# Kernel tuning notes

Measured on AMD Instinct MI355X. Metric: run time of the kernel, lower is better.

The kernel has to match this reference:

```python
import jax, jax.numpy as jnp
import numpy as np

B, C, H, W = 16, 128, 64, 64
LN_EPS = 1e-5


def _gru_dir(x, w_ih, w_hh, b_ih, b_hh, reverse):
    # x: [N, T, C]; PyTorch GRU cell math:
    # r = sig(Wir x + bir + Whr h + bhr); z = sig(Wiz x + biz + Whz h + bhz)
    xp = jnp.einsum('ntc,gc->ntg', x, w_ih) + b_ih  # [N,T,3C] precomputed input gates
    xs = jnp.swapaxes(xp, 0, 1)  # [T,N,3C]
    h0 = jnp.zeros((x.shape[0], w_hh.shape[1]), x.dtype)

    def step(h, xt):
        g = h @ w_hh.T + b_hh
        xr, xz, xn = jnp.split(xt, 3, axis=-1)
        hr, hz, hn = jnp.split(g, 3, axis=-1)
        r = jax.nn.sigmoid(xr + hr)
        z = jax.nn.sigmoid(xz + hz)
        n = jnp.tanh(xn + r * hn)
        h2 = (1.0 - z) * n + z * h
        return h2, h2

    _, ys = jax.lax.scan(step, h0, xs, reverse=reverse)
    return jnp.swapaxes(ys, 0, 1)  # [N,T,C]


def _gru_bidir(x, wih_f, whh_f, bih_f, bhh_f, wih_b, whh_b, bib_b, bhh_b):
    of = _gru_dir(x, wih_f, whh_f, bih_f, bhh_f, False)
    ob = _gru_dir(x, wih_b, whh_b, bib_b, bhh_b, True)
    return jnp.concatenate([of, ob], axis=-1)  # [N,T,2C]


def _forward(x, ln_g, ln_b,
             h_wih_f, h_whh_f, h_bih_f, h_bhh_f,
             h_wih_b, h_whh_b, h_bih_b, h_bhh_b,
             w_wih_f, w_whh_f, w_bih_f, w_bhh_f,
             w_wih_b, w_whh_b, w_bih_b, w_bhh_b,
             proj_w, proj_b):
    Bn, Cc, Hh, Ww = x.shape
    x_flat = x.reshape(Bn, Cc, Hh * Ww).transpose(0, 2, 1)  # b (h w) c
    mu = x_flat.mean(-1, keepdims=True)
    var = ((x_flat - mu) ** 2).mean(-1, keepdims=True)
    xn = (x_flat - mu) * jax.lax.rsqrt(var + LN_EPS) * ln_g + ln_b
    x4 = xn.reshape(Bn, Hh, Ww, Cc)
    # horizontal scan: rows as batch, sequence along W
    x_h = x4.reshape(Bn * Hh, Ww, Cc)
    out_h = _gru_bidir(x_h, h_wih_f, h_whh_f, h_bih_f, h_bhh_f,
                       h_wih_b, h_whh_b, h_bih_b, h_bhh_b)
    out_h = out_h.reshape(Bn, Hh * Ww, 2 * Cc)
    # vertical scan: cols as batch, sequence along H
    x_v = x4.transpose(0, 2, 1, 3).reshape(Bn * Ww, Hh, Cc)
    out_v = _gru_bidir(x_v, w_wih_f, w_whh_f, w_bih_f, w_bhh_f,
                       w_wih_b, w_whh_b, w_bih_b, w_bhh_b)
    out_v = out_v.reshape(Bn, Ww, Hh, 2 * Cc).transpose(0, 2, 1, 3).reshape(Bn, Hh * Ww, 2 * Cc)
    out = jnp.concatenate([out_h, out_v], axis=-1) @ proj_w.T + proj_b
    out = out + x_flat  # dropout in eval mode = identity
    return out.transpose(0, 2, 1).reshape(Bn, Cc, Hh, Ww)


def setup_inputs():
    key = jax.random.key(0)
    key, kx = jax.random.split(key)
    d = {
        'x': jax.random.normal(kx, (B, C, H, W), jnp.float32),
        'ln_g': jnp.ones((C,), jnp.float32),
        'ln_b': jnp.zeros((C,), jnp.float32),
    }
    bound = 1.0 / np.sqrt(C)  # torch GRU init: U(-1/sqrt(hidden), 1/sqrt(hidden))
    shapes = {'wih': (3 * C, C), 'whh': (3 * C, C), 'bih': (3 * C,), 'bhh': (3 * C,)}
    for pre in ('h', 'w'):
        for dr in ('f', 'b'):
            for p, sh in shapes.items():
                key, k1 = jax.random.split(key)
                d[f'{pre}_{p}_{dr}'] = jax.random.uniform(k1, sh, jnp.float32, -bound, bound)
    bp = 1.0 / np.sqrt(4 * C)
    key, k1, k2 = jax.random.split(key, 3)
    d['proj_w'] = jax.random.uniform(k1, (C, 4 * C), jnp.float32, -bp, bp)
    d['proj_b'] = jax.random.uniform(k2, (C,), jnp.float32, -bp, bp)
    return d


def reference(x, ln_g, ln_b,
              h_wih_f, h_whh_f, h_bih_f, h_bhh_f,
              h_wih_b, h_whh_b, h_bih_b, h_bhh_b,
              w_wih_f, w_whh_f, w_bih_f, w_bhh_f,
              w_wih_b, w_whh_b, w_bih_b, w_bhh_b,
              proj_w, proj_b):
    return _forward(x, ln_g, ln_b,
                    h_wih_f, h_whh_f, h_bih_f, h_bhh_f,
                    h_wih_b, h_whh_b, h_bih_b, h_bhh_b,
                    w_wih_f, w_whh_f, w_bih_f, w_bhh_f,
                    w_wih_b, w_whh_b, w_bih_b, w_bhh_b,
                    proj_w, proj_b)
```

## Files before the change

### kernel.cpp

```cpp
#include <hip/hip_runtime.h>

typedef short bf16x8 __attribute__((ext_vector_type(8)));
typedef float f32x4 __attribute__((ext_vector_type(4)));

static __device__ __forceinline__ unsigned short f2bf(float f) {
  unsigned u = __builtin_bit_cast(unsigned, f);
  u += 0x7FFFu + ((u >> 16) & 1u);
  return (unsigned short)(u >> 16);
}

static __device__ __forceinline__ bf16x8 pack8s(const float* p, float s) {
  float4 a = *(const float4*)p;
  float4 b = *(const float4*)(p + 4);
  bf16x8 r;
  r[0] = (short)f2bf(a.x * s); r[1] = (short)f2bf(a.y * s);
  r[2] = (short)f2bf(a.z * s); r[3] = (short)f2bf(a.w * s);
  r[4] = (short)f2bf(b.x * s); r[5] = (short)f2bf(b.y * s);
  r[6] = (short)f2bf(b.z * s); r[7] = (short)f2bf(b.w * s);
  return r;
}

#define NLOG2E -1.442695040888963f
#define N2LOG2E -2.885390081777927f

__global__ __launch_bounds__(512, 2) void ln_kernel(
    const float* __restrict__ x, const float* __restrict__ lg,
    const float* __restrict__ lb, unsigned short* __restrict__ xn,
    const float* __restrict__ pw, unsigned short* __restrict__ pwb) {
  __shared__ __align__(16) unsigned char slds[35840];
  float* mu_s = (float*)(slds + 34816);
  float* rs_s = (float*)(slds + 35328);
  const int tid = threadIdx.x;
  const int bid = blockIdx.x;
  if (bid < 128) {
    const int i = bid * 512 + tid;
    pwb[i] = f2bf(pw[i]);
  }
  const int b = bid >> 5;
  const int hw0 = (bid & 31) << 7;
  const int q = tid >> 5, slot = tid & 31;
  const int lane = tid & 63, wv = tid >> 6;

  const float* xbase = x + ((size_t)b * 128) * 4096 + hw0 + (slot << 2);
  float4 xv[8];
#pragma unroll
  for (int p = 0; p < 8; ++p)
    xv[p] = *(const float4*)(xbase + (size_t)(q * 8 + p) * 4096);

  float s1[4] = {0.f, 0.f, 0.f, 0.f}, s2[4] = {0.f, 0.f, 0.f, 0.f};
#pragma unroll
  for (int p = 0; p < 8; ++p) {
    s1[0] += xv[p].x; s2[0] = fmaf(xv[p].x, xv[p].x, s2[0]);
    s1[1] += xv[p].y; s2[1] = fmaf(xv[p].y, xv[p].y, s2[1]);
    s1[2] += xv[p].z; s2[2] = fmaf(xv[p].z, xv[p].z, s2[2]);
    s1[3] += xv[p].w; s2[3] = fmaf(xv[p].w, xv[p].w, s2[3]);
  }
#pragma unroll
  for (int j = 0; j < 4; ++j) {
    s1[j] += __shfl_xor(s1[j], 32);
    s2[j] += __shfl_xor(s2[j], 32);
  }
  if (lane < 32) {
    float* psp = (float*)(slds + (wv * 32 + slot) * 36);
#pragma unroll
    for (int j = 0; j < 4; ++j) { psp[j] = s1[j]; psp[4 + j] = s2[j]; }
  }
  __syncthreads();
  if (tid < 128) {
    const int sl2 = tid >> 2, j2 = tid & 3;
    float a1 = 0.f, a2 = 0.f;
#pragma unroll
    for (int w = 0; w < 8; ++w) {
      const float* psp = (const float*)(slds + (w * 32 + sl2) * 36);
      a1 += psp[j2]; a2 += psp[4 + j2];
    }
    const float mu = a1 * 0.0078125f;
    const float var = a2 * 0.0078125f - mu * mu;
    mu_s[tid] = mu;
    rs_s[tid] = rsqrtf(var + 1e-5f);
  }
  __syncthreads();

  float lgv[8], lbv[8];
#pragma unroll
  for (int p = 0; p < 8; ++p) { lgv[p] = lg[q * 8 + p]; lbv[p] = lb[q * 8 + p]; }
#pragma unroll
  for (int j = 0; j < 4; ++j) {
    const int pos = (slot << 2) + j;
    const float mu = mu_s[pos], rs = rs_s[pos];
    float y[8];
#pragma unroll
    for (int p = 0; p < 8; ++p) {
      const float xvj = j == 0 ? xv[p].x : j == 1 ? xv[p].y : j == 2 ? xv[p].z : xv[p].w;
      y[p] = (xvj - mu) * rs * lgv[p] + lbv[p];
    }
    unsigned h0, h1, h2, h3;
    asm("v_cvt_pk_bf16_f32 %0, %1, %2" : "=v"(h0) : "v"(y[0]), "v"(y[1]));
    asm("v_cvt_pk_bf16_f32 %0, %1, %2" : "=v"(h1) : "v"(y[2]), "v"(y[3]));
    asm("v_cvt_pk_bf16_f32 %0, %1, %2" : "=v"(h2) : "v"(y[4]), "v"(y[5]));
    asm("v_cvt_pk_bf16_f32 %0, %1, %2" : "=v"(h3) : "v"(y[6]), "v"(y[7]));
    uint4 v; v.x = h0; v.y = h1; v.z = h2; v.w = h3;
    *(uint4*)(slds + pos * 272 + (q << 4)) = v;
  }
  __syncthreads();
#pragma unroll
  for (int it = 0; it < 4; ++it) {
    const int idx = (it << 9) + tid;
    const int row = idx >> 4, g = idx & 15;
    uint4 v = *(const uint4*)(slds + row * 272 + (g << 4));
    *(uint4*)((unsigned char*)xn + ((size_t)(b * 4096 + hw0 + row)) * 256 + (g << 4)) = v;
  }
}

__global__ __launch_bounds__(512, 2) void scan_kernel(
    const unsigned short* __restrict__ xn, unsigned short* __restrict__ cat,
    const float* __restrict__ wih0, const float* __restrict__ whh0,
    const float* __restrict__ bih0, const float* __restrict__ bhh0,
    const float* __restrict__ wih1, const float* __restrict__ whh1,
    const float* __restrict__ bih1, const float* __restrict__ bhh1,
    const float* __restrict__ wih2, const float* __restrict__ whh2,
    const float* __restrict__ bih2, const float* __restrict__ bhh2,
    const float* __restrict__ wih3, const float* __restrict__ whh3,
    const float* __restrict__ bih3, const float* __restrict__ bhh3) {
  __shared__ __align__(16) unsigned char lds[16384];
  const int tid = threadIdx.x;
  const int bid = blockIdx.x;
  const int dir = bid >> 6;
  const int grp = bid & 63;
  const int fwd = !(dir & 1);
  const int vert = dir >> 1;
  const int b = grp >> 2;
  const int r0 = (grp & 3) << 4;
  const int wv = tid >> 6;
  const int lane = tid & 63;
  const int l15 = lane & 15;
  const int l4 = lane >> 4;

  const float* wih = dir == 0 ? wih0 : dir == 1 ? wih1 : dir == 2 ? wih2 : wih3;
  const float* whh = dir == 0 ? whh0 : dir == 1 ? whh1 : dir == 2 ? whh2 : whh3;
  const float* bih = dir == 0 ? bih0 : dir == 1 ? bih1 : dir == 2 ? bih2 : bih3;
  const float* bhh = dir == 0 ? bhh0 : dir == 1 ? bhh1 : dir == 2 ? bhh2 : bhh3;

  const int ca = (wv << 4) + l15;
  bf16x8 wf[3][2][4];
#pragma unroll
  for (int g = 0; g < 3; ++g) {
    const float sc = g == 2 ? N2LOG2E : NLOG2E;
#pragma unroll
    for (int s = 0; s < 2; ++s) {
      const float* Wp = s ? whh : wih;
#pragma unroll
      for (int kc = 0; kc < 4; ++kc)
        wf[g][s][kc] = pack8s(Wp + (size_t)((g << 7) + ca) * 128 + (kc << 5) + (l4 << 3), sc);
    }
  }
  const int cb = (wv << 4) + (l4 << 2);
  f32x4 br4, bz4, bnx4, bnh4;
  {
    float4 a = *(const float4*)(bih + cb), b2 = *(const float4*)(bhh + cb);
    br4[0] = (a.x + b2.x) * NLOG2E; br4[1] = (a.y + b2.y) * NLOG2E;
    br4[2] = (a.z + b2.z) * NLOG2E; br4[3] = (a.w + b2.w) * NLOG2E;
    a = *(const float4*)(bih + 128 + cb); b2 = *(const float4*)(bhh + 128 + cb);
    bz4[0] = (a.x + b2.x) * NLOG2E; bz4[1] = (a.y + b2.y) * NLOG2E;
    bz4[2] = (a.z + b2.z) * NLOG2E; bz4[3] = (a.w + b2.w) * NLOG2E;
    a = *(const float4*)(bih + 256 + cb);
    bnx4[0] = a.x * N2LOG2E; bnx4[1] = a.y * N2LOG2E;
    bnx4[2] = a.z * N2LOG2E; bnx4[3] = a.w * N2LOG2E;
    b2 = *(const float4*)(bhh + 256 + cb);
    bnh4[0] = b2.x * N2LOG2E; bnh4[1] = b2.y * N2LOG2E;
    bnh4[2] = b2.z * N2LOG2E; bnh4[3] = b2.w * N2LOG2E;
  }

  const int ss = tid >> 4, ck = tid & 15;
  const unsigned char* xsp =
      (const unsigned char*)xn +
      (vert ? ((size_t)b << 20) + (size_t)(r0 + ss) * 256 + (ck << 4)
            : ((size_t)(b * 64 + r0 + ss) << 14) + (ck << 4));
  const int xstep = vert ? 16384 : 256;
  const int sdst = (ss * 256 + (ck << 4)) ^ ((ss & 15) << 4);

  const int seq = r0 + l15;
  const int cstep = vert ? 65536 : 1024;
  unsigned char* catp =
      (unsigned char*)cat +
      ((size_t)b * 4096 + (size_t)(vert ? seq : seq * 64)) * 1024 + dir * 256 + (cb << 1) +
      (size_t)(fwd ? 0 : 63) * cstep;
  const int cdelta = fwd ? cstep : -cstep;

  *(unsigned long long*)(lds + 8192 + tid * 8) = 0ull;
  f32x4 hst = {0.f, 0.f, 0.f, 0.f};

  uint4 sX, sY;
  f32x4 grA, gzA, gnxA, grB, gzB, gnxB;
  {
    const unsigned char* xlq =
        (const unsigned char*)xn +
        (vert ? ((size_t)b << 20) + (size_t)(fwd ? 0 : 63) * 16384 + (size_t)seq * 256
              : ((size_t)(b * 64 + seq) << 14) + (size_t)(fwd ? 0 : 63) * 256) +
        (l4 << 4);
    bf16x8 x0[4];
#pragma unroll
    for (int kc = 0; kc < 4; ++kc) x0[kc] = *(const bf16x8*)(xlq + (kc << 6));
    uint4 s1v;
    if (tid < 256) {
      s1v = *(const uint4*)(xsp + (fwd ? 1 : 62) * xstep);
      sX = *(const uint4*)(xsp + (fwd ? 2 : 61) * xstep);
    }
    grA = br4; gzA = bz4; gnxA = bnx4;
#pragma unroll
    for (int kc = 0; kc < 4; ++kc) {
      grA = __builtin_amdgcn_mfma_f32_16x16x32_bf16(wf[0][0][kc], x0[kc], grA, 0, 0, 0);
      gzA = __builtin_amdgcn_mfma_f32_16x16x32_bf16(wf[1][0][kc], x0[kc], gzA, 0, 0, 0);
      gnxA = __builtin_amdgcn_mfma_f32_16x16x32_bf16(wf[2][0][kc], x0[kc], gnxA, 0, 0, 0);
    }
    if (tid < 256) *(uint4*)(lds + 4096 + sdst) = s1v;
  }
  __syncthreads();

#define STEP(TT, HCUR, HNXT, XRD, XWR, XW, XL, GRC, GZC, GNXC, GRN, GZN, GNXN)  \
  {                                                                             \
    bf16x8 ha[4], xa[4];                                                        \
    _Pragma("unroll")                                                           \
    for (int kc = 0; kc < 4; ++kc) {                                            \
      const int base = (l15 * 256 + (kc << 6) + (l4 << 4)) ^ (l15 << 4);        \
      ha[kc] = *(const bf16x8*)(lds + (HCUR) + base);                           \
      xa[kc] = *(const bf16x8*)(lds + (XRD) + base);                            \
    }                                                                           \
    if (tid < 256) {                                                            \
      *(uint4*)(lds + (XWR) + sdst) = XW;                                       \
      const int tl = (TT) + 3 > 63 ? 63 : (TT) + 3;                             \
      XL = *(const uint4*)(xsp + (fwd ? tl : 63 - tl) * xstep);                 \
    }                                                                           \
    f32x4 rh = {0.f, 0.f, 0.f, 0.f}, zh = {0.f, 0.f, 0.f, 0.f}, nh = bnh4;     \
    _Pragma("unroll")                                                           \
    for (int kc = 0; kc < 4; ++kc) {                                            \
      rh = __builtin_amdgcn_mfma_f32_16x16x32_bf16(wf[0][1][kc], ha[kc], rh, 0, 0, 0); \
      zh = __builtin_amdgcn_mfma_f32_16x16x32_bf16(wf[1][1][kc], ha[kc], zh, 0, 0, 0); \
      nh = __builtin_amdgcn_mfma_f32_16x16x32_bf16(wf[2][1][kc], ha[kc], nh, 0, 0, 0); \
    }                                                                           \
    GRN = br4; GZN = bz4; GNXN = bnx4;                                          \
    _Pragma("unroll")                                                           \
    for (int kc = 0; kc < 4; ++kc) {                                            \
      GRN = __builtin_amdgcn_mfma_f32_16x16x32_bf16(wf[0][0][kc], xa[kc], GRN, 0, 0, 0); \
      GZN = __builtin_amdgcn_mfma_f32_16x16x32_bf16(wf[1][0][kc], xa[kc], GZN, 0, 0, 0); \
      GNXN = __builtin_amdgcn_mfma_f32_16x16x32_bf16(wf[2][0][kc], xa[kc], GNXN, 0, 0, 0); \
    }                                                                           \
    f32x4 hnew;                                                                 \
    _Pragma("unroll")                                                           \
    for (int r = 0; r < 4; ++r) {                                               \
      const float er = __builtin_amdgcn_exp2f(GRC[r] + rh[r]);                  \
      const float rr = __builtin_amdgcn_rcpf(1.f + er);                         \
      const float ez = __builtin_amdgcn_exp2f(GZC[r] + zh[r]);                  \
      const float zz = __builtin_amdgcn_rcpf(1.f + ez);                         \
      const float pre = GNXC[r] + rr * nh[r];                                   \
      const float e2 = __builtin_amdgcn_exp2f(pre);                             \
      const float nn = fmaf(2.f, __builtin_amdgcn_rcpf(1.f + e2), -1.f);        \
      hnew[r] = nn + zz * (hst[r] - nn);                                        \
    }                                                                           \
    hst = hnew;                                                                 \
    unsigned hp0, hp1;                                                          \
    asm("v_cvt_pk_bf16_f32 %0, %1, %2" : "=v"(hp0) : "v"(hnew[0]), "v"(hnew[1])); \
    asm("v_cvt_pk_bf16_f32 %0, %1, %2" : "=v"(hp1) : "v"(hnew[2]), "v"(hnew[3])); \
    {                                                                           \
      unsigned long long hp = (unsigned long long)hp0 | ((unsigned long long)hp1 << 32); \
      *(unsigned long long*)(lds + (HNXT) + ((l15 * 256 + (cb << 1)) ^ (l15 << 4))) = hp; \
    }                                                                           \
    {                                                                           \
      uint2 v; v.x = hp0; v.y = hp1;                                            \
      *(uint2*)catp = v;                                                        \
      catp += cdelta;                                                           \
    }                                                                           \
    asm volatile("s_waitcnt lgkmcnt(0)" ::: "memory");                          \
    __builtin_amdgcn_s_barrier();                                               \
    asm volatile("" ::: "memory");                                              \
  }

  for (int tt2 = 0; tt2 < 64; tt2 += 2) {
    STEP(tt2, 8192, 12288, 4096, 0, sX, sY, grA, gzA, gnxA, grB, gzB, gnxB);
    STEP(tt2 + 1, 12288, 8192, 0, 4096, sY, sX, grB, gzB, gnxB, grA, gzA, gnxA);
  }
#undef STEP
}

__global__ __launch_bounds__(512, 4) void proj_kernel(
    const unsigned short* __restrict__ cat, const unsigned short* __restrict__ pwb,
    const float* __restrict__ pb, const float* __restrict__ x,
    float* __restrict__ out) {
  __shared__ __align__(16) unsigned char lds[33280];
  const int tid = threadIdx.x;
  const int bid = blockIdx.x;
  const int row0 = bid << 6;
  const int b = row0 >> 12;
  const int hw0 = row0 & 4095;
  const int wv = tid >> 6, lane = tid & 63, l15 = lane & 15, l4 = lane >> 4;

  const int cc = (wv << 4) + l15;
  bf16x8 wfr[16];
#pragma unroll
  for (int kc = 0; kc < 16; ++kc)
    wfr[kc] = *(const bf16x8*)(pwb + (size_t)cc * 512 + (kc << 5) + (l4 << 3));
  const float pbv = pb[cc];

  f32x4 acc[4];
#pragma unroll
  for (int mt = 0; mt < 4; ++mt) acc[mt] = {pbv, pbv, pbv, pbv};

#pragma unroll
  for (int s = 0; s < 2; ++s) {
#pragma unroll
    for (int it = 0; it < 4; ++it) {
      const int item = tid + (it << 9);
      const int rr = item >> 6, ckk = item & 63;
      uint4 v = *(const uint4*)((const unsigned char*)cat +
                                ((size_t)(row0 + (s << 5) + rr)) * 1024 + ckk * 16);
      *(uint4*)(lds + rr * 1024 + ((ckk ^ (rr & 7)) << 4)) = v;
    }
    __syncthreads();
#pragma unroll
    for (int mh = 0; mh < 2; ++mh) {
      const int mt = (s << 1) + mh;
      const int rl = (mh << 4) + l15;
#pragma unroll
      for (int kc = 0; kc < 16; ++kc) {
        bf16x8 af =
            *(const bf16x8*)(lds + rl * 1024 + ((((kc << 2) + l4) ^ (rl & 7)) << 4));
        acc[mt] = __builtin_amdgcn_mfma_f32_16x16x32_bf16(af, wfr[kc], acc[mt], 0, 0, 0);
      }
    }
    __syncthreads();
  }

#pragma unroll
  for (int mt = 0; mt < 4; ++mt)
#pragma unroll
    for (int j = 0; j < 4; ++j)
      *(float*)(lds + cc * 260 + (((mt << 4) + (l4 << 2) + j) << 2)) = acc[mt][j];
  __syncthreads();
#pragma unroll
  for (int it = 0; it < 16; ++it) {
    const int c = (wv << 4) + it;
    const float v = *(const float*)(lds + c * 260 + (lane << 2));
    const size_t off = (size_t)(b * 128 + c) * 4096 + hw0 + lane;
    out[off] = v + x[off];
  }
}

extern "C" void kernel_launch(void* const* d_in, const int* in_sizes, int n_in,
                              void* d_out, int out_size, void* d_ws, size_t ws_size,
                              hipStream_t stream) {
  const float* x = (const float*)d_in[0];
  const float* lg = (const float*)d_in[1];
  const float* lb = (const float*)d_in[2];
  unsigned short* xn = (unsigned short*)d_ws;
  unsigned short* cat =
      (unsigned short*)((unsigned char*)d_ws + 16777216);
  unsigned short* pwb =
      (unsigned short*)((unsigned char*)d_ws + 16777216 + 67108864);

  ln_kernel<<<512, 512, 0, stream>>>(x, lg, lb, xn, (const float*)d_in[19], pwb);
  scan_kernel<<<256, 512, 0, stream>>>(
      xn, cat,
      (const float*)d_in[3], (const float*)d_in[4], (const float*)d_in[5], (const float*)d_in[6],
      (const float*)d_in[7], (const float*)d_in[8], (const float*)d_in[9], (const float*)d_in[10],
      (const float*)d_in[11], (const float*)d_in[12], (const float*)d_in[13], (const float*)d_in[14],
      (const float*)d_in[15], (const float*)d_in[16], (const float*)d_in[17], (const float*)d_in[18]);
  proj_kernel<<<1024, 512, 0, stream>>>(cat, pwb, (const float*)d_in[20], x,
                                        (float*)d_out);
}
```

Before: 114.2 us.

## Store GRU outputs and projection weights in fp8 and use fp8 MFMA

The scan kernel now writes the bidirectional GRU outputs as fp8 instead of bf16, which halves the intermediate buffer. The projection kernel reads this fp8 data along with fp8-converted projection weights and uses the 16x16x32 fp8 MFMA. The aim is to cut global memory traffic for the large concatenated buffer and the LDS footprint in the projection. It risks accuracy loss from fp8 (e4m3) quantisation of both activations and weights, which may exceed tolerance.

```diff
diff --git a/kernel.cpp b/kernel.cpp
--- a/kernel.cpp
+++ b/kernel.cpp
@@ -26,15 +26,19 @@
 __global__ __launch_bounds__(512, 2) void ln_kernel(
     const float* __restrict__ x, const float* __restrict__ lg,
     const float* __restrict__ lb, unsigned short* __restrict__ xn,
-    const float* __restrict__ pw, unsigned short* __restrict__ pwb) {
+    const float* __restrict__ pw, unsigned char* __restrict__ pwb) {
   __shared__ __align__(16) unsigned char slds[35840];
   float* mu_s = (float*)(slds + 34816);
   float* rs_s = (float*)(slds + 35328);
   const int tid = threadIdx.x;
   const int bid = blockIdx.x;
-  if (bid < 128) {
-    const int i = bid * 512 + tid;
-    pwb[i] = f2bf(pw[i]);
+  if (bid < 32) {
+    const int i = ((bid << 9) + tid) << 2;
+    float4 v = *(const float4*)(pw + i);
+    unsigned lo8, hi8;
+    asm("v_cvt_pk_fp8_f32 %0, %1, %2" : "=v"(lo8) : "v"(v.x), "v"(v.y));
+    asm("v_cvt_pk_fp8_f32 %0, %1, %2" : "=v"(hi8) : "v"(v.z), "v"(v.w));
+    *(unsigned*)(pwb + i) = (lo8 & 0xffffu) | (hi8 << 16);
   }
   const int b = bid >> 5;
   const int hw0 = (bid & 31) << 7;
@@ -113,7 +117,7 @@
 }
 
 __global__ __launch_bounds__(512, 2) void scan_kernel(
-    const unsigned short* __restrict__ xn, unsigned short* __restrict__ cat,
+    const unsigned short* __restrict__ xn, unsigned char* __restrict__ cat,
     const float* __restrict__ wih0, const float* __restrict__ whh0,
     const float* __restrict__ bih0, const float* __restrict__ bhh0,
     const float* __restrict__ wih1, const float* __restrict__ whh1,
@@ -180,10 +184,9 @@
   const int sdst = (ss * 256 + (ck << 4)) ^ ((ss & 15) << 4);
 
   const int seq = r0 + l15;
-  const int cstep = vert ? 65536 : 1024;
+  const int cstep = vert ? 32768 : 512;
   unsigned char* catp =
-      (unsigned char*)cat +
-      ((size_t)b * 4096 + (size_t)(vert ? seq : seq * 64)) * 1024 + dir * 256 + (cb << 1) +
+      cat + ((size_t)b * 4096 + (size_t)(vert ? seq : seq * 64)) * 512 + dir * 128 + cb +
       (size_t)(fwd ? 0 : 63) * cstep;
   const int cdelta = fwd ? cstep : -cstep;
 
@@ -266,8 +269,10 @@
       *(unsigned long long*)(lds + (HNXT) + ((l15 * 256 + (cb << 1)) ^ (l15 << 4))) = hp; \
     }                                                                           \
     {                                                                           \
-      uint2 v; v.x = hp0; v.y = hp1;                                            \
-      *(uint2*)catp = v;                                                        \
+      unsigned lo8, hi8;                                                        \
+      asm("v_cvt_pk_fp8_f32 %0, %1, %2" : "=v"(lo8) : "v"(hnew[0]), "v"(hnew[1])); \
+      asm("v_cvt_pk_fp8_f32 %0, %1, %2" : "=v"(hi8) : "v"(hnew[2]), "v"(hnew[3])); \
+      *(unsigned*)catp = (lo8 & 0xffffu) | (hi8 << 16);                         \
       catp += cdelta;                                                           \
     }                                                                           \
     asm volatile("s_waitcnt lgkmcnt(0)" ::: "memory");                          \
@@ -283,7 +288,7 @@
 }
 
 __global__ __launch_bounds__(512, 4) void proj_kernel(
-    const unsigned short* __restrict__ cat, const unsigned short* __restrict__ pwb,
+    const unsigned char* __restrict__ cat, const unsigned char* __restrict__ pwb,
     const float* __restrict__ pb, const float* __restrict__ x,
     float* __restrict__ out) {
   __shared__ __align__(16) unsigned char lds[33280];
@@ -295,10 +300,10 @@
   const int wv = tid >> 6, lane = tid & 63, l15 = lane & 15, l4 = lane >> 4;
 
   const int cc = (wv << 4) + l15;
-  bf16x8 wfr[16];
+  long wfr[16];
 #pragma unroll
   for (int kc = 0; kc < 16; ++kc)
-    wfr[kc] = *(const bf16x8*)(pwb + (size_t)cc * 512 + (kc << 5) + (l4 << 3));
+    wfr[kc] = *(const long*)(pwb + (size_t)cc * 512 + (kc << 5) + (l4 << 3));
   const float pbv = pb[cc];
 
   f32x4 acc[4];
@@ -308,12 +313,11 @@
 #pragma unroll
   for (int s = 0; s < 2; ++s) {
 #pragma unroll
-    for (int it = 0; it < 4; ++it) {
+    for (int it = 0; it < 2; ++it) {
       const int item = tid + (it << 9);
-      const int rr = item >> 6, ckk = item & 63;
-      uint4 v = *(const uint4*)((const unsigned char*)cat +
-                                ((size_t)(row0 + (s << 5) + rr)) * 1024 + ckk * 16);
-      *(uint4*)(lds + rr * 1024 + ((ckk ^ (rr & 7)) << 4)) = v;
+      const int rr = item >> 5, ckk = item & 31;
+      uint4 v = *(const uint4*)(cat + ((size_t)(row0 + (s << 5) + rr)) * 512 + (ckk << 4));
+      *(uint4*)(lds + rr * 512 + ((ckk ^ (rr & 7)) << 4)) = v;
     }
     __syncthreads();
 #pragma unroll
@@ -322,9 +326,10 @@
       const int rl = (mh << 4) + l15;
 #pragma unroll
       for (int kc = 0; kc < 16; ++kc) {
-        bf16x8 af =
-            *(const bf16x8*)(lds + rl * 1024 + ((((kc << 2) + l4) ^ (rl & 7)) << 4));
-        acc[mt] = __builtin_amdgcn_mfma_f32_16x16x32_bf16(af, wfr[kc], acc[mt], 0, 0, 0);
+        const int g8 = (kc << 2) + l4;
+        long af = *(const long*)(lds + rl * 512 +
+                                 ((((g8 >> 1) ^ (rl & 7)) << 4) | ((g8 & 1) << 3)));
+        acc[mt] = __builtin_amdgcn_mfma_f32_16x16x32_fp8_fp8(af, wfr[kc], acc[mt], 0, 0, 0);
       }
     }
     __syncthreads();
@@ -352,10 +357,8 @@
   const float* lg = (const float*)d_in[1];
   const float* lb = (const float*)d_in[2];
   unsigned short* xn = (unsigned short*)d_ws;
-  unsigned short* cat =
-      (unsigned short*)((unsigned char*)d_ws + 16777216);
-  unsigned short* pwb =
-      (unsigned short*)((unsigned char*)d_ws + 16777216 + 67108864);
+  unsigned char* cat = (unsigned char*)d_ws + 16777216;
+  unsigned char* pwb = (unsigned char*)d_ws + 16777216 + 33554432;
 
   ln_kernel<<<512, 512, 0, stream>>>(x, lg, lb, xn, (const float*)d_in[19], pwb);
   scan_kernel<<<256, 512, 0, stream>>>(
```

Result: faster. 101.5 us (-11.2%).
